# Performance work log

Measured on AMD Instinct MI355X. Metric: run time of the kernel, lower is better.

## Reference

```python
import jax, jax.numpy as jnp
import numpy as np

TOP_K = 2  # config.num_active_experts


def setup_inputs() -> dict:
    key = jax.random.key(0)
    k1, k2, k3, k4 = jax.random.split(key, 4)
    B, S, D = 2, 2048, 1024
    E, W = 8, 1024  # 8 experts, each width 1024 -> total_expert_width = 8192
    x = jax.random.normal(k1, (B, S, D), dtype=jnp.float32)
    router_w = jax.random.normal(k2, (E, D), dtype=jnp.float32) * 0.02
    w1 = jax.random.normal(k3, (D, E * W), dtype=jnp.float32) * 0.02
    w2 = jax.random.normal(k4, (E * W, D), dtype=jnp.float32) * 0.02
    return {"x": x, "router_w": router_w, "w1": w1, "w2": w2}


def reference(x, router_w, w1, w2):
    B, S, D = x.shape
    E = router_w.shape[0]
    W = w1.shape[1] // E  # uniform expert width
    T = B * S
    xf = x.reshape(T, D)

    # Router: sigmoid gating, top-k, sum-normalized weights (norm_topk_prob)
    router_logits = jnp.einsum('td,ed->te', xf, router_w)
    router_probs = jax.nn.sigmoid(router_logits.astype(jnp.float32))
    top_w, sel = jax.lax.top_k(router_probs, TOP_K)          # [T,K]
    top_w = top_w / (top_w.sum(axis=-1, keepdims=True) + 1e-20)
    top_w = top_w.astype(x.dtype)

    # Expert MLPs: expert e uses w1[:, off_e:off_e+W], w2[off_e:off_e+W, :].
    # Uniform width -> single batched einsum over experts (same math as the
    # padded-gather / block-sparse SDD/DSD grouped GEMM pipeline).
    W1e = w1.reshape(D, E, W).transpose(1, 0, 2)             # [E,D,W]
    W2e = w2.reshape(E, W, D)                                # [E,W,D]
    h = jnp.einsum('td,edw->etw', xf, W1e)                   # up-proj
    a = jnp.square(jax.nn.relu(h))                           # relu_squared
    y = jnp.einsum('etw,ewd->etd', a, W2e)                   # down-proj

    # Weighted scatter-combine: combine_weights[t,e] = top_w if e selected else 0
    cw = jnp.zeros((T, E), dtype=x.dtype).at[jnp.arange(T)[:, None], sel].set(top_w)
    out = jnp.einsum('etd,te->td', y, cw)
    return out.reshape(B, S, D)
```

## Files before the change

kernel.cpp:

```cpp
#include <hip/hip_runtime.h>
#include <hip/hip_bf16.h>


#define T_TOKENS 4096
#define DD 1024
#define EE 8
#define WW 1024
#define CAP 2048
#define BM 128
#define BN 128
#define BK 32
#define MT (CAP / BM)
#define NT 8

typedef short bf16x8 __attribute__((ext_vector_type(8)));
typedef float f32x4 __attribute__((ext_vector_type(4)));

__device__ __forceinline__ void gload_lds16(const void* g, void* l) {
  __builtin_amdgcn_global_load_lds((__attribute__((address_space(1))) void*)(g),
                                   (__attribute__((address_space(3))) void*)(l),
                                   16, 0, 0);
}

__global__ __launch_bounds__(256) void transpose_cvt(
    const float* __restrict__ src, __hip_bfloat16* __restrict__ dst,
    int src_ld, int dst_ld, long src_blk, long dst_blk)
{
  __shared__ float tile[32][33];
  const float* s = src + (long)blockIdx.z * src_blk;
  __hip_bfloat16* d = dst + (long)blockIdx.z * dst_blk;
  int tx = threadIdx.x, ty = threadIdx.y;
  int c0 = blockIdx.x * 32;
  int r0 = blockIdx.y * 32;
#pragma unroll
  for (int i = 0; i < 4; i++)
    tile[ty + 8 * i][tx] = s[(long)(c0 + ty + 8 * i) * src_ld + r0 + tx];
  __syncthreads();
#pragma unroll
  for (int i = 0; i < 4; i++)
    d[(long)(r0 + ty + 8 * i) * dst_ld + c0 + tx] =
        __float2bfloat16(tile[tx][ty + 8 * i]);
}

__global__ __launch_bounds__(256) void router_kernel(
    const float* __restrict__ x, const float* __restrict__ rw,
    __hip_bfloat16* __restrict__ xb, int* __restrict__ sel,
    float* __restrict__ wpair)
{
  int lane = threadIdx.x & 63;
  int wave = threadIdx.x >> 6;
  int t = blockIdx.x * 4 + wave;
  const float* xrow = x + (size_t)t * DD;
  float acc[EE];
#pragma unroll
  for (int e = 0; e < EE; e++) acc[e] = 0.f;
#pragma unroll
  for (int i = 0; i < DD / 64; i++) {
    int d = lane + i * 64;
    float xv = xrow[d];
    xb[t * DD + d] = __float2bfloat16(xv);
#pragma unroll
    for (int e = 0; e < EE; e++) acc[e] += xv * rw[e * DD + d];
  }
#pragma unroll
  for (int e = 0; e < EE; e++) {
#pragma unroll
    for (int off = 32; off > 0; off >>= 1)
      acc[e] += __shfl_down(acc[e], off, 64);
  }
  if (lane == 0) {
    float p[EE];
#pragma unroll
    for (int e = 0; e < EE; e++) p[e] = 1.f / (1.f + expf(-acc[e]));
    int e0 = 0; float b0 = p[0];
    for (int e = 1; e < EE; e++) if (p[e] > b0) { b0 = p[e]; e0 = e; }
    int e1 = -1; float b1 = -1.f;
    for (int e = 0; e < EE; e++) {
      if (e == e0) continue;
      if (p[e] > b1) { b1 = p[e]; e1 = e; }
    }
    float s = b0 + b1 + 1e-20f;
    sel[t] = e0 | (e1 << 8);
    wpair[2 * t]     = b0 / s;
    wpair[2 * t + 1] = b1 / s;
  }
}

__global__ __launch_bounds__(1024) void build_lists(
    const int* __restrict__ sel, const float* __restrict__ wpair,
    int* __restrict__ counts, int* __restrict__ idx, float* __restrict__ aw)
{
  __shared__ int lcnt[EE];
  int tid = threadIdx.x;
  if (tid < EE) lcnt[tid] = 0;
  __syncthreads();
#pragma unroll
  for (int j = 0; j < T_TOKENS / 1024; j++) {
    int t = j * 1024 + tid;
    int s = sel[t];
    int e0 = s & 0xff, e1 = (s >> 8) & 0xff;
    float w0 = wpair[2 * t], w1 = wpair[2 * t + 1];
    int s0 = atomicAdd(&lcnt[e0], 1);
    idx[e0 * CAP + s0] = t;  aw[e0 * CAP + s0] = w0;
    int s1 = atomicAdd(&lcnt[e1], 1);
    idx[e1 * CAP + s1] = t;  aw[e1 * CAP + s1] = w1;
  }
  __syncthreads();
  if (tid < EE) counts[tid] = lcnt[tid];
}

__global__ __launch_bounds__(256) void gemm1_kernel(
    const __hip_bfloat16* __restrict__ xb, const __hip_bfloat16* __restrict__ w1t,
    const int* __restrict__ counts, const int* __restrict__ idx,
    __hip_bfloat16* __restrict__ act)
{
  __shared__ short As[BM * BK];
  __shared__ short Bs[BN * BK];
  int b = blockIdx.x;
  int e = b / (MT * NT);
  int rem = b % (MT * NT);
  int mt = rem / NT, nt = rem % NT;
  int n_e = counts[e];
  if (mt * BM >= n_e) return;

  int tid = threadIdx.x;
  int lane = tid & 63;
  int wave = __builtin_amdgcn_readfirstlane(tid >> 6);
  int wm = (wave >> 1) * 64, wn = (wave & 1) * 64;
  int m16 = lane & 15, qd = lane >> 4;

  const __hip_bfloat16* gA[2];
  const __hip_bfloat16* gB[2];
#pragma unroll
  for (int i = 0; i < 2; i++) {
    int sg = i * 256 + tid;
    int r = sg >> 2;
    int q = (sg & 3) ^ ((r >> 1) & 3);
    int rowA = mt * BM + r;
    int slot = rowA < n_e ? rowA : n_e - 1;
    int tok = idx[e * CAP + slot];
    gA[i] = xb + tok * DD + q * 8;
    gB[i] = w1t + (e * WW + nt * BN + r) * DD + q * 8;
  }
  short* ldsA0 = As + (wave * 64) * 8;
  short* ldsA1 = As + (256 + wave * 64) * 8;
  short* ldsB0 = Bs + (wave * 64) * 8;
  short* ldsB1 = Bs + (256 + wave * 64) * 8;

  int aoff[4], boff[4];
#pragma unroll
  for (int i = 0; i < 4; i++) {
    int ra = wm + i * 16 + m16;
    aoff[i] = (ra * 4 + (qd ^ ((ra >> 1) & 3))) * 8;
    int rb = wn + i * 16 + m16;
    boff[i] = (rb * 4 + (qd ^ ((rb >> 1) & 3))) * 8;
  }

  f32x4 zero = {0.f, 0.f, 0.f, 0.f};
  f32x4 acc[4][4];
#pragma unroll
  for (int mi = 0; mi < 4; mi++)
#pragma unroll
    for (int ni = 0; ni < 4; ni++) acc[mi][ni] = zero;

  for (int k0 = 0; k0 < DD; k0 += BK) {
    gload_lds16(gA[0] + k0, ldsA0);
    gload_lds16(gA[1] + k0, ldsA1);
    gload_lds16(gB[0] + k0, ldsB0);
    gload_lds16(gB[1] + k0, ldsB1);
    __syncthreads();
    bf16x8 af[4], bfr[4];
#pragma unroll
    for (int i = 0; i < 4; i++) af[i] = *(const bf16x8*)(As + aoff[i]);
#pragma unroll
    for (int i = 0; i < 4; i++) bfr[i] = *(const bf16x8*)(Bs + boff[i]);
#pragma unroll
    for (int mi = 0; mi < 4; mi++)
#pragma unroll
      for (int ni = 0; ni < 4; ni++)
        acc[mi][ni] = __builtin_amdgcn_mfma_f32_16x16x32_bf16(
            af[mi], bfr[ni], acc[mi][ni], 0, 0, 0);
    __syncthreads();
  }

#pragma unroll
  for (int mi = 0; mi < 4; mi++) {
#pragma unroll
    for (int reg = 0; reg < 4; reg++) {
      int rowt = mt * BM + wm + mi * 16 + qd * 4 + reg;
      if (rowt < n_e) {
#pragma unroll
        for (int ni = 0; ni < 4; ni++) {
          float v = acc[mi][ni][reg];
          v = v > 0.f ? v * v : 0.f;
          int col = nt * BN + wn + ni * 16 + m16;
          act[(e * CAP + rowt) * WW + col] = __float2bfloat16(v);
        }
      }
    }
  }
}

__global__ __launch_bounds__(256) void gemm2_kernel(
    const __hip_bfloat16* __restrict__ act, const __hip_bfloat16* __restrict__ w2t,
    const int* __restrict__ counts, const int* __restrict__ idx,
    const float* __restrict__ aw, float* __restrict__ out)
{
  __shared__ short As[BM * BK];
  __shared__ short Bs[BN * BK];
  int b = blockIdx.x;
  int e = b / (MT * NT);
  int rem = b % (MT * NT);
  int mt = rem / NT, nt = rem % NT;
  int n_e = counts[e];
  if (mt * BM >= n_e) return;

  int tid = threadIdx.x;
  int lane = tid & 63;
  int wave = __builtin_amdgcn_readfirstlane(tid >> 6);
  int wm = (wave >> 1) * 64, wn = (wave & 1) * 64;
  int m16 = lane & 15, qd = lane >> 4;

  const __hip_bfloat16* gA[2];
  const __hip_bfloat16* gB[2];
#pragma unroll
  for (int i = 0; i < 2; i++) {
    int sg = i * 256 + tid;
    int r = sg >> 2;
    int q = (sg & 3) ^ ((r >> 1) & 3);
    gA[i] = act + (e * CAP + mt * BM + r) * WW + q * 8;
    gB[i] = w2t + (e * DD + nt * BN + r) * WW + q * 8;
  }
  short* ldsA0 = As + (wave * 64) * 8;
  short* ldsA1 = As + (256 + wave * 64) * 8;
  short* ldsB0 = Bs + (wave * 64) * 8;
  short* ldsB1 = Bs + (256 + wave * 64) * 8;

  int aoff[4], boff[4];
#pragma unroll
  for (int i = 0; i < 4; i++) {
    int ra = wm + i * 16 + m16;
    aoff[i] = (ra * 4 + (qd ^ ((ra >> 1) & 3))) * 8;
    int rb = wn + i * 16 + m16;
    boff[i] = (rb * 4 + (qd ^ ((rb >> 1) & 3))) * 8;
  }

  f32x4 zero = {0.f, 0.f, 0.f, 0.f};
  f32x4 acc[4][4];
#pragma unroll
  for (int mi = 0; mi < 4; mi++)
#pragma unroll
    for (int ni = 0; ni < 4; ni++) acc[mi][ni] = zero;

  for (int k0 = 0; k0 < WW; k0 += BK) {
    gload_lds16(gA[0] + k0, ldsA0);
    gload_lds16(gA[1] + k0, ldsA1);
    gload_lds16(gB[0] + k0, ldsB0);
    gload_lds16(gB[1] + k0, ldsB1);
    __syncthreads();
    bf16x8 af[4], bfr[4];
#pragma unroll
    for (int i = 0; i < 4; i++) af[i] = *(const bf16x8*)(As + aoff[i]);
#pragma unroll
    for (int i = 0; i < 4; i++) bfr[i] = *(const bf16x8*)(Bs + boff[i]);
#pragma unroll
    for (int mi = 0; mi < 4; mi++)
#pragma unroll
      for (int ni = 0; ni < 4; ni++)
        acc[mi][ni] = __builtin_amdgcn_mfma_f32_16x16x32_bf16(
            af[mi], bfr[ni], acc[mi][ni], 0, 0, 0);
    __syncthreads();
  }

#pragma unroll
  for (int mi = 0; mi < 4; mi++) {
#pragma unroll
    for (int reg = 0; reg < 4; reg++) {
      int slot = mt * BM + wm + mi * 16 + qd * 4 + reg;
      if (slot < n_e) {
        int tok = idx[e * CAP + slot];
        float wv = aw[e * CAP + slot];
#pragma unroll
        for (int ni = 0; ni < 4; ni++) {
          int col = nt * BN + wn + ni * 16 + m16;
          atomicAdd(out + tok * DD + col, acc[mi][ni][reg] * wv);
        }
      }
    }
  }
}

extern "C" void kernel_launch(void* const* d_in, const int* in_sizes, int n_in,
                              void* d_out, int out_size, void* d_ws, size_t ws_size,
                              hipStream_t stream)
{
  const float* x  = (const float*)d_in[0];
  const float* rw = (const float*)d_in[1];
  const float* w1 = (const float*)d_in[2];
  const float* w2 = (const float*)d_in[3];
  float* out = (float*)d_out;

  char* ws = (char*)d_ws;
  __hip_bfloat16* xb  = (__hip_bfloat16*)ws;  ws += (size_t)T_TOKENS * DD * 2;
  __hip_bfloat16* w1t = (__hip_bfloat16*)ws;  ws += (size_t)EE * WW * DD * 2;
  __hip_bfloat16* w2t = (__hip_bfloat16*)ws;  ws += (size_t)EE * DD * WW * 2;
  __hip_bfloat16* act = (__hip_bfloat16*)ws;  ws += (size_t)EE * CAP * WW * 2;
  int*   counts = (int*)ws;                   ws += 256;
  int*   idx    = (int*)ws;                   ws += (size_t)EE * CAP * 4;
  float* aw     = (float*)ws;                 ws += (size_t)EE * CAP * 4;
  int*   sel    = (int*)ws;                   ws += (size_t)T_TOKENS * 4;
  float* wpair  = (float*)ws;                 ws += (size_t)T_TOKENS * 8;

  hipMemsetAsync(d_out, 0, (size_t)out_size * 4, stream);

  dim3 tb(32, 8);
  transpose_cvt<<<dim3(DD / 32, (EE * WW) / 32, 1), tb, 0, stream>>>(
      w1, w1t, EE * WW, DD, 0, 0);
  transpose_cvt<<<dim3(WW / 32, DD / 32, EE), tb, 0, stream>>>(
      w2, w2t, DD, WW, (long)WW * DD, (long)DD * WW);

  router_kernel<<<T_TOKENS / 4, 256, 0, stream>>>(x, rw, xb, sel, wpair);
  build_lists<<<1, 1024, 0, stream>>>(sel, wpair, counts, idx, aw);
  gemm1_kernel<<<EE * MT * NT, 256, 0, stream>>>(xb, w1t, counts, idx, act);
  gemm2_kernel<<<EE * MT * NT, 256, 0, stream>>>(act, w2t, counts, idx, aw, out);
}
```

Baseline: 228.2 us.

## Replace atomic scatter with per-expert output buffer plus combine kernel; shrink BN; vectorize transpose

The down-projection now writes bf16 per-slot expert outputs to a buffer instead of atomically adding weighted rows into the output. A new combine kernel gathers each token's two expert rows and writes the weighted sum, which also removes the output memset. The GEMM tile N is halved to 64, doubling the block count for better CU occupancy. The weight transpose kernel moves to 64x64 tiles with vectorized loads and stores. The cost is extra traffic for the intermediate y buffer, one more launch, and bf16 rounding of expert outputs before the combine.

```diff
diff --git a/kernel.cpp b/kernel.cpp
--- a/kernel.cpp
+++ b/kernel.cpp
@@ -8,10 +8,10 @@
 #define WW 1024
 #define CAP 2048
 #define BM 128
-#define BN 128
+#define BN 64
 #define BK 32
 #define MT (CAP / BM)
-#define NT 8
+#define NT 16
 
 typedef short bf16x8 __attribute__((ext_vector_type(8)));
 typedef float f32x4 __attribute__((ext_vector_type(4)));
@@ -22,24 +22,40 @@
                                    16, 0, 0);
 }
 
+__device__ __forceinline__ float bf2f(unsigned short u) {
+  union { unsigned int i; float f; } v; v.i = (unsigned int)u << 16; return v.f;
+}
+
 __global__ __launch_bounds__(256) void transpose_cvt(
     const float* __restrict__ src, __hip_bfloat16* __restrict__ dst,
     int src_ld, int dst_ld, long src_blk, long dst_blk)
 {
-  __shared__ float tile[32][33];
+  __shared__ float tile[64][65];
   const float* s = src + (long)blockIdx.z * src_blk;
   __hip_bfloat16* d = dst + (long)blockIdx.z * dst_blk;
-  int tx = threadIdx.x, ty = threadIdx.y;
-  int c0 = blockIdx.x * 32;
-  int r0 = blockIdx.y * 32;
-#pragma unroll
-  for (int i = 0; i < 4; i++)
-    tile[ty + 8 * i][tx] = s[(long)(c0 + ty + 8 * i) * src_ld + r0 + tx];
+  int tx = threadIdx.x;
+  int ty = threadIdx.y;
+  int c0 = blockIdx.x * 64;
+  int r0 = blockIdx.y * 64;
+#pragma unroll
+  for (int i = 0; i < 4; i++) {
+    int sr = ty + 16 * i;
+    f32x4 v = *(const f32x4*)(s + (long)(c0 + sr) * src_ld + r0 + tx * 4);
+    tile[sr][tx * 4 + 0] = v[0];
+    tile[sr][tx * 4 + 1] = v[1];
+    tile[sr][tx * 4 + 2] = v[2];
+    tile[sr][tx * 4 + 3] = v[3];
+  }
   __syncthreads();
 #pragma unroll
-  for (int i = 0; i < 4; i++)
-    d[(long)(r0 + ty + 8 * i) * dst_ld + c0 + tx] =
-        __float2bfloat16(tile[tx][ty + 8 * i]);
+  for (int i = 0; i < 4; i++) {
+    int dr = ty + 16 * i;
+    union { __hip_bfloat16 hb[4]; ushort4 u4; } pk;
+#pragma unroll
+    for (int j = 0; j < 4; j++)
+      pk.hb[j] = __float2bfloat16(tile[tx * 4 + j][dr]);
+    *(ushort4*)((unsigned short*)d + (long)(r0 + dr) * dst_ld + c0 + tx * 4) = pk.u4;
+  }
 }
 
 __global__ __launch_bounds__(256) void router_kernel(
@@ -87,8 +103,8 @@
 }
 
 __global__ __launch_bounds__(1024) void build_lists(
-    const int* __restrict__ sel, const float* __restrict__ wpair,
-    int* __restrict__ counts, int* __restrict__ idx, float* __restrict__ aw)
+    const int* __restrict__ sel, int* __restrict__ counts,
+    int* __restrict__ idx, int* __restrict__ tslot)
 {
   __shared__ int lcnt[EE];
   int tid = threadIdx.x;
@@ -99,11 +115,12 @@
     int t = j * 1024 + tid;
     int s = sel[t];
     int e0 = s & 0xff, e1 = (s >> 8) & 0xff;
-    float w0 = wpair[2 * t], w1 = wpair[2 * t + 1];
     int s0 = atomicAdd(&lcnt[e0], 1);
-    idx[e0 * CAP + s0] = t;  aw[e0 * CAP + s0] = w0;
+    idx[e0 * CAP + s0] = t;
     int s1 = atomicAdd(&lcnt[e1], 1);
-    idx[e1 * CAP + s1] = t;  aw[e1 * CAP + s1] = w1;
+    idx[e1 * CAP + s1] = t;
+    tslot[2 * t]     = e0 * CAP + s0;
+    tslot[2 * t + 1] = e1 * CAP + s1;
   }
   __syncthreads();
   if (tid < EE) counts[tid] = lcnt[tid];
@@ -126,11 +143,11 @@
   int tid = threadIdx.x;
   int lane = tid & 63;
   int wave = __builtin_amdgcn_readfirstlane(tid >> 6);
-  int wm = (wave >> 1) * 64, wn = (wave & 1) * 64;
+  int wm = (wave >> 1) * 64, wn = (wave & 1) * 32;
   int m16 = lane & 15, qd = lane >> 4;
 
   const __hip_bfloat16* gA[2];
-  const __hip_bfloat16* gB[2];
+  const __hip_bfloat16* gB;
 #pragma unroll
   for (int i = 0; i < 2; i++) {
     int sg = i * 256 + tid;
@@ -140,44 +157,49 @@
     int slot = rowA < n_e ? rowA : n_e - 1;
     int tok = idx[e * CAP + slot];
     gA[i] = xb + tok * DD + q * 8;
-    gB[i] = w1t + (e * WW + nt * BN + r) * DD + q * 8;
+  }
+  {
+    int r = tid >> 2;
+    int q = (tid & 3) ^ ((r >> 1) & 3);
+    gB = w1t + (e * WW + nt * BN + r) * DD + q * 8;
   }
   short* ldsA0 = As + (wave * 64) * 8;
   short* ldsA1 = As + (256 + wave * 64) * 8;
-  short* ldsB0 = Bs + (wave * 64) * 8;
-  short* ldsB1 = Bs + (256 + wave * 64) * 8;
-
-  int aoff[4], boff[4];
+  short* ldsB  = Bs + (wave * 64) * 8;
+
+  int aoff[4], boff[2];
 #pragma unroll
   for (int i = 0; i < 4; i++) {
     int ra = wm + i * 16 + m16;
     aoff[i] = (ra * 4 + (qd ^ ((ra >> 1) & 3))) * 8;
+  }
+#pragma unroll
+  for (int i = 0; i < 2; i++) {
     int rb = wn + i * 16 + m16;
     boff[i] = (rb * 4 + (qd ^ ((rb >> 1) & 3))) * 8;
   }
 
   f32x4 zero = {0.f, 0.f, 0.f, 0.f};
-  f32x4 acc[4][4];
+  f32x4 acc[4][2];
 #pragma unroll
   for (int mi = 0; mi < 4; mi++)
 #pragma unroll
-    for (int ni = 0; ni < 4; ni++) acc[mi][ni] = zero;
+    for (int ni = 0; ni < 2; ni++) acc[mi][ni] = zero;
 
   for (int k0 = 0; k0 < DD; k0 += BK) {
     gload_lds16(gA[0] + k0, ldsA0);
     gload_lds16(gA[1] + k0, ldsA1);
-    gload_lds16(gB[0] + k0, ldsB0);
-    gload_lds16(gB[1] + k0, ldsB1);
+    gload_lds16(gB + k0, ldsB);
     __syncthreads();
-    bf16x8 af[4], bfr[4];
+    bf16x8 af[4], bfr[2];
 #pragma unroll
     for (int i = 0; i < 4; i++) af[i] = *(const bf16x8*)(As + aoff[i]);
 #pragma unroll
-    for (int i = 0; i < 4; i++) bfr[i] = *(const bf16x8*)(Bs + boff[i]);
+    for (int i = 0; i < 2; i++) bfr[i] = *(const bf16x8*)(Bs + boff[i]);
 #pragma unroll
     for (int mi = 0; mi < 4; mi++)
 #pragma unroll
-      for (int ni = 0; ni < 4; ni++)
+      for (int ni = 0; ni < 2; ni++)
         acc[mi][ni] = __builtin_amdgcn_mfma_f32_16x16x32_bf16(
             af[mi], bfr[ni], acc[mi][ni], 0, 0, 0);
     __syncthreads();
@@ -190,7 +212,7 @@
       int rowt = mt * BM + wm + mi * 16 + qd * 4 + reg;
       if (rowt < n_e) {
 #pragma unroll
-        for (int ni = 0; ni < 4; ni++) {
+        for (int ni = 0; ni < 2; ni++) {
           float v = acc[mi][ni][reg];
           v = v > 0.f ? v * v : 0.f;
           int col = nt * BN + wn + ni * 16 + m16;
@@ -203,8 +225,7 @@
 
 __global__ __launch_bounds__(256) void gemm2_kernel(
     const __hip_bfloat16* __restrict__ act, const __hip_bfloat16* __restrict__ w2t,
-    const int* __restrict__ counts, const int* __restrict__ idx,
-    const float* __restrict__ aw, float* __restrict__ out)
+    const int* __restrict__ counts, __hip_bfloat16* __restrict__ y)
 {
   __shared__ short As[BM * BK];
   __shared__ short Bs[BN * BK];
@@ -218,55 +239,60 @@
   int tid = threadIdx.x;
   int lane = tid & 63;
   int wave = __builtin_amdgcn_readfirstlane(tid >> 6);
-  int wm = (wave >> 1) * 64, wn = (wave & 1) * 64;
+  int wm = (wave >> 1) * 64, wn = (wave & 1) * 32;
   int m16 = lane & 15, qd = lane >> 4;
 
   const __hip_bfloat16* gA[2];
-  const __hip_bfloat16* gB[2];
+  const __hip_bfloat16* gB;
 #pragma unroll
   for (int i = 0; i < 2; i++) {
     int sg = i * 256 + tid;
     int r = sg >> 2;
     int q = (sg & 3) ^ ((r >> 1) & 3);
     gA[i] = act + (e * CAP + mt * BM + r) * WW + q * 8;
-    gB[i] = w2t + (e * DD + nt * BN + r) * WW + q * 8;
+  }
+  {
+    int r = tid >> 2;
+    int q = (tid & 3) ^ ((r >> 1) & 3);
+    gB = w2t + (e * DD + nt * BN + r) * WW + q * 8;
   }
   short* ldsA0 = As + (wave * 64) * 8;
   short* ldsA1 = As + (256 + wave * 64) * 8;
-  short* ldsB0 = Bs + (wave * 64) * 8;
-  short* ldsB1 = Bs + (256 + wave * 64) * 8;
-
-  int aoff[4], boff[4];
+  short* ldsB  = Bs + (wave * 64) * 8;
+
+  int aoff[4], boff[2];
 #pragma unroll
   for (int i = 0; i < 4; i++) {
     int ra = wm + i * 16 + m16;
     aoff[i] = (ra * 4 + (qd ^ ((ra >> 1) & 3))) * 8;
+  }
+#pragma unroll
+  for (int i = 0; i < 2; i++) {
     int rb = wn + i * 16 + m16;
     boff[i] = (rb * 4 + (qd ^ ((rb >> 1) & 3))) * 8;
   }
 
   f32x4 zero = {0.f, 0.f, 0.f, 0.f};
-  f32x4 acc[4][4];
+  f32x4 acc[4][2];
 #pragma unroll
   for (int mi = 0; mi < 4; mi++)
 #pragma unroll
-    for (int ni = 0; ni < 4; ni++) acc[mi][ni] = zero;
+    for (int ni = 0; ni < 2; ni++) acc[mi][ni] = zero;
 
   for (int k0 = 0; k0 < WW; k0 += BK) {
     gload_lds16(gA[0] + k0, ldsA0);
     gload_lds16(gA[1] + k0, ldsA1);
-    gload_lds16(gB[0] + k0, ldsB0);
-    gload_lds16(gB[1] + k0, ldsB1);
+    gload_lds16(gB + k0, ldsB);
     __syncthreads();
-    bf16x8 af[4], bfr[4];
+    bf16x8 af[4], bfr[2];
 #pragma unroll
     for (int i = 0; i < 4; i++) af[i] = *(const bf16x8*)(As + aoff[i]);
 #pragma unroll
-    for (int i = 0; i < 4; i++) bfr[i] = *(const bf16x8*)(Bs + boff[i]);
+    for (int i = 0; i < 2; i++) bfr[i] = *(const bf16x8*)(Bs + boff[i]);
 #pragma unroll
     for (int mi = 0; mi < 4; mi++)
 #pragma unroll
-      for (int ni = 0; ni < 4; ni++)
+      for (int ni = 0; ni < 2; ni++)
         acc[mi][ni] = __builtin_amdgcn_mfma_f32_16x16x32_bf16(
             af[mi], bfr[ni], acc[mi][ni], 0, 0, 0);
     __syncthreads();
@@ -278,16 +304,33 @@
     for (int reg = 0; reg < 4; reg++) {
       int slot = mt * BM + wm + mi * 16 + qd * 4 + reg;
       if (slot < n_e) {
-        int tok = idx[e * CAP + slot];
-        float wv = aw[e * CAP + slot];
-#pragma unroll
-        for (int ni = 0; ni < 4; ni++) {
+#pragma unroll
+        for (int ni = 0; ni < 2; ni++) {
           int col = nt * BN + wn + ni * 16 + m16;
-          atomicAdd(out + tok * DD + col, acc[mi][ni][reg] * wv);
+          y[(e * CAP + slot) * DD + col] = __float2bfloat16(acc[mi][ni][reg]);
         }
       }
     }
   }
+}
+
+__global__ __launch_bounds__(256) void combine_kernel(
+    const __hip_bfloat16* __restrict__ y, const int* __restrict__ tslot,
+    const float* __restrict__ wpair, float* __restrict__ out)
+{
+  int t = blockIdx.x;
+  int c = threadIdx.x * 4;
+  int s0 = tslot[2 * t], s1 = tslot[2 * t + 1];
+  float w0 = wpair[2 * t], w1 = wpair[2 * t + 1];
+  const unsigned short* yu = (const unsigned short*)y;
+  ushort4 a = *(const ushort4*)(yu + (size_t)s0 * DD + c);
+  ushort4 bq = *(const ushort4*)(yu + (size_t)s1 * DD + c);
+  f32x4 o;
+  o[0] = w0 * bf2f(a.x) + w1 * bf2f(bq.x);
+  o[1] = w0 * bf2f(a.y) + w1 * bf2f(bq.y);
+  o[2] = w0 * bf2f(a.z) + w1 * bf2f(bq.z);
+  o[3] = w0 * bf2f(a.w) + w1 * bf2f(bq.w);
+  *(f32x4*)(out + (size_t)t * DD + c) = o;
 }
 
 extern "C" void kernel_launch(void* const* d_in, const int* in_sizes, int n_in,
@@ -305,22 +348,22 @@
   __hip_bfloat16* w1t = (__hip_bfloat16*)ws;  ws += (size_t)EE * WW * DD * 2;
   __hip_bfloat16* w2t = (__hip_bfloat16*)ws;  ws += (size_t)EE * DD * WW * 2;
   __hip_bfloat16* act = (__hip_bfloat16*)ws;  ws += (size_t)EE * CAP * WW * 2;
+  __hip_bfloat16* y   = (__hip_bfloat16*)ws;  ws += (size_t)EE * CAP * DD * 2;
   int*   counts = (int*)ws;                   ws += 256;
   int*   idx    = (int*)ws;                   ws += (size_t)EE * CAP * 4;
-  float* aw     = (float*)ws;                 ws += (size_t)EE * CAP * 4;
   int*   sel    = (int*)ws;                   ws += (size_t)T_TOKENS * 4;
+  int*   tslot  = (int*)ws;                   ws += (size_t)T_TOKENS * 8;
   float* wpair  = (float*)ws;                 ws += (size_t)T_TOKENS * 8;
 
-  hipMemsetAsync(d_out, 0, (size_t)out_size * 4, stream);
-
-  dim3 tb(32, 8);
-  transpose_cvt<<<dim3(DD / 32, (EE * WW) / 32, 1), tb, 0, stream>>>(
+  dim3 tb(16, 16);
+  transpose_cvt<<<dim3(DD / 64, (EE * WW) / 64, 1), tb, 0, stream>>>(
       w1, w1t, EE * WW, DD, 0, 0);
-  transpose_cvt<<<dim3(WW / 32, DD / 32, EE), tb, 0, stream>>>(
+  transpose_cvt<<<dim3(WW / 64, DD / 64, EE), tb, 0, stream>>>(
       w2, w2t, DD, WW, (long)WW * DD, (long)DD * WW);
 
   router_kernel<<<T_TOKENS / 4, 256, 0, stream>>>(x, rw, xb, sel, wpair);
-  build_lists<<<1, 1024, 0, stream>>>(sel, wpair, counts, idx, aw);
+  build_lists<<<1, 1024, 0, stream>>>(sel, counts, idx, tslot);
   gemm1_kernel<<<EE * MT * NT, 256, 0, stream>>>(xb, w1t, counts, idx, act);
-  gemm2_kernel<<<EE * MT * NT, 256, 0, stream>>>(act, w2t, counts, idx, aw, out);
-}
+  gemm2_kernel<<<EE * MT * NT, 256, 0, stream>>>(act, w2t, counts, y);
+  combine_kernel<<<T_TOKENS, 256, 0, stream>>>(y, tslot, wpair, out);
+}
```

Measured after the change: 220.4 us. -3.4%, faster.
